# Kernel tuning notes

Measured on AMD Instinct MI355X. Metric: run time of the kernel, lower is better.

The kernel has to match this reference:

```python
import jax, jax.numpy as jnp
import numpy as np

B = 1; S = 2048; HID = 1024; NH = 8; HD = 128; INTER = 4096
EPS = 1e-6; THETA = 10000.0


def rms_norm(x, w):
    # Gemma RMSNorm: x * rsqrt(mean(x^2)+eps) * (1 + w)
    v = jnp.mean(x * x, axis=-1, keepdims=True)
    return x * jax.lax.rsqrt(v + EPS) * (1.0 + w)


def rope_cos_sin(seqlen):
    inv = 1.0 / (THETA ** (jnp.arange(0, HD, 2, dtype=jnp.float32) / HD))
    t = jnp.arange(seqlen, dtype=jnp.float32)
    f = jnp.outer(t, inv)                       # (S, HD/2)
    emb = jnp.concatenate([f, f], axis=-1)      # (S, HD)
    return jnp.cos(emb), jnp.sin(emb)


def rotate_half(x):
    x1, x2 = jnp.split(x, 2, axis=-1)
    return jnp.concatenate([-x2, x1], axis=-1)


def apply_rope(x, cos, sin):
    return x * cos[None, None] + rotate_half(x) * sin[None, None]


def expert_forward(x, mask, params):
    """One GemmaDecoderLayer; returns output plus PRE-RoPE q/k/v (as the torch module exposes)."""
    w_ln, wq, wk, wv, wo, w_pln, wg, wu, wd = params
    res = x
    h = rms_norm(x, w_ln)

    def proj(w):
        return (h @ w).reshape(B, -1, NH, HD).transpose(0, 2, 1, 3)  # (B,H,S,D)

    q, k, v = proj(wq), proj(wk), proj(wv)      # stored before rotary in the original
    cos, sin = rope_cos_sin(x.shape[1])
    qr, kr = apply_rope(q, cos, sin), apply_rope(k, cos, sin)
    scores = jnp.einsum('bhqd,bhkd->bhqk', qr, kr) * (HD ** -0.5) + mask
    attn = jnp.einsum('bhqk,bhkd->bhqd', jax.nn.softmax(scores, axis=-1), v)
    attn = attn.transpose(0, 2, 1, 3).reshape(B, -1, NH * HD) @ wo
    h1 = res + attn
    m = rms_norm(h1, w_pln)
    mlp = (jax.nn.gelu(m @ wg, approximate=True) * (m @ wu)) @ wd  # gelu_pytorch_tanh
    return h1 + mlp, q, k, v


def setup_inputs() -> dict:
    key = jax.random.key(0)
    ks = iter(jax.random.split(key, 40))

    def w(shape, scale=0.02):
        return jax.random.normal(next(ks), shape, jnp.float32) * scale

    inp = {
        'x_a': jax.random.normal(next(ks), (B, S, HID), jnp.float32),
        'x_b': jax.random.normal(next(ks), (B, S, HID), jnp.float32),
    }
    tri = jnp.tril(jnp.ones((S, S), bool))
    causal = jnp.where(tri, 0.0, -1e9).astype(jnp.float32)[None, None]  # additive causal mask
    inp['mask_a'] = causal
    inp['mask_b'] = causal
    inp['mix_mask'] = jnp.zeros((B, 1, 2 * S, 2 * S), jnp.float32)      # non-causal cross-expert
    for e in ('a', 'b'):
        inp['w_ln_' + e] = jnp.zeros((HID,), jnp.float32)
        inp['w_q_' + e] = w((HID, NH * HD))
        inp['w_k_' + e] = w((HID, NH * HD))
        inp['w_v_' + e] = w((HID, NH * HD))
        inp['w_o_' + e] = w((NH * HD, HID))
        inp['w_pln_' + e] = jnp.zeros((HID,), jnp.float32)
        inp['w_g_' + e] = w((HID, INTER))
        inp['w_u_' + e] = w((HID, INTER))
        inp['w_d_' + e] = w((INTER, HID))
    return inp


def reference(x_a, x_b, mask_a, mask_b, mix_mask,
              w_ln_a, w_q_a, w_k_a, w_v_a, w_o_a, w_pln_a, w_g_a, w_u_a, w_d_a,
              w_ln_b, w_q_b, w_k_b, w_v_b, w_o_b, w_pln_b, w_g_b, w_u_b, w_d_b):
    pa = (w_ln_a, w_q_a, w_k_a, w_v_a, w_o_a, w_pln_a, w_g_a, w_u_a, w_d_a)
    pb = (w_ln_b, w_q_b, w_k_b, w_v_b, w_o_b, w_pln_b, w_g_b, w_u_b, w_d_b)
    out_a, qa, ka, va = expert_forward(x_a, mask_a, pa)
    out_b, qb, kb, vb = expert_forward(x_b, mask_b, pb)
    # cross-expert mixed attention over concatenated (pre-RoPE) streams
    q = jnp.concatenate([qa, qb], axis=2)
    k = jnp.concatenate([ka, kb], axis=2)
    v = jnp.concatenate([va, vb], axis=2)
    scores = jnp.einsum('bhqd,bhkd->bhqk', q, k) * (HD ** -0.5) + mix_mask
    mixed = jnp.einsum('bhqk,bhkd->bhqd', jax.nn.softmax(scores, axis=-1), v)
    mixed = mixed.transpose(0, 2, 1, 3).reshape(B, 2 * S, NH * HD)
    ma, mb = mixed[:, :S], mixed[:, S:]
    return jnp.stack([out_a + ma @ w_o_a, out_b + mb @ w_o_b])
```

## Files before the change

kernel.cpp:

```cpp
#include <hip/hip_runtime.h>
#include <hip/hip_bf16.h>
#include <math.h>

#define S 2048
#define HID 1024
#define NH 8
#define HD 128
#define INTER 4096
#define EPSV 1e-6f
#define THETA 10000.0f

typedef __hip_bfloat16 bf16;
typedef unsigned short u16;
typedef __attribute__((ext_vector_type(8))) short bf16x8;
typedef __attribute__((ext_vector_type(4))) float f32x4;

__device__ inline float bu2f(u16 u) {
    unsigned int x = ((unsigned int)u) << 16;
    return __uint_as_float(x);
}
__device__ inline u16 f2bu(float f) {
    bf16 h = __float2bfloat16(f);
    return *reinterpret_cast<u16*>(&h);
}
__device__ inline float ldin(const void* p, size_t i, bool isbf) {
    return isbf ? bu2f(((const u16*)p)[i]) : ((const float*)p)[i];
}
__device__ inline float gelu_tanh(float x) {
    float x3 = x * x * x;
    return 0.5f * x * (1.f + tanhf(0.7978845608028654f * (x + 0.044715f * x3)));
}
__device__ inline void gload16(const u16* g, u16* l) {
    __builtin_amdgcn_global_load_lds(
        (const __attribute__((address_space(1))) void*)g,
        (__attribute__((address_space(3))) void*)l, 16, 0, 0);
}

__global__ __launch_bounds__(256) void probe_kernel(const unsigned short* __restrict__ x,
                                                    int* __restrict__ flag) {
    __shared__ int red[256];
    int tid = threadIdx.x;
    int cnt = 0;
    for (int i = tid; i < 2048; i += 256) {
        unsigned short u = x[2 * i];
        int e = (u >> 7) & 0xFF;
        cnt += (e >= 110 && e <= 135) ? 1 : 0;
    }
    red[tid] = cnt;
    __syncthreads();
    for (int off = 128; off > 0; off >>= 1) {
        if (tid < off) red[tid] += red[tid + off];
        __syncthreads();
    }
    if (tid == 0) *flag = (red[0] > 1024) ? 1 : 0;
}

__global__ __launch_bounds__(256) void transpose_w(const void* __restrict__ W,
                                                   u16* __restrict__ WT,
                                                   const int* __restrict__ flag,
                                                   int K, int N) {
    bool isbf = (*flag != 0);
    __shared__ float t[32][33];
    int n0 = blockIdx.x * 32, k0 = blockIdx.y * 32;
    int c = threadIdx.x & 31, r = threadIdx.x >> 5;
#pragma unroll
    for (int p = 0; p < 4; p++)
        t[r + 8 * p][c] = ldin(W, (size_t)(k0 + r + 8 * p) * N + n0 + c, isbf);
    __syncthreads();
#pragma unroll
    for (int p = 0; p < 4; p++) {
        int row = r + 8 * p;
        WT[(size_t)(n0 + row) * K + k0 + c] = f2bu(t[c][row]);
    }
}

__global__ __launch_bounds__(256) void transpose_v(const u16* __restrict__ V0,
                                                   const u16* __restrict__ V1, int sv,
                                                   u16* __restrict__ VT) {
    const u16* V = blockIdx.z ? V1 : V0;
    VT += (size_t)blockIdx.z * ((size_t)NH * HD * S);
    __shared__ u16 t[32][33];
    int k0 = blockIdx.x * 32;
    int d0 = blockIdx.y * 32;
    int c = threadIdx.x & 31, r = threadIdx.x >> 5;
#pragma unroll
    for (int p = 0; p < 4; p++)
        t[r + 8 * p][c] = V[(size_t)(k0 + r + 8 * p) * sv + d0 + c];
    __syncthreads();
#pragma unroll
    for (int p = 0; p < 4; p++)
        VT[(size_t)(d0 + r + 8 * p) * S + k0 + c] = t[c][r + 8 * p];
}

struct RmsDual {
    const void* x[2];
    const void* w[2];
    u16* y[2];
};
__global__ __launch_bounds__(256) void rmsnorm_kernel(RmsDual rd,
                                                      const int* __restrict__ flag,
                                                      int dual) {
    int e = blockIdx.y;
    const void* x = rd.x[e];
    const void* w = rd.w[e];
    u16* y = rd.y[e];
    bool isbf = (*flag != 0);
    bool xbf = dual && isbf;
    int row = blockIdx.x;
    size_t base = (size_t)row * HID;
    __shared__ float red[256];
    float xv[4];
    float s = 0.f;
#pragma unroll
    for (int i = 0; i < 4; i++) {
        float v = ldin(x, base + threadIdx.x + 256 * i, xbf);
        xv[i] = v;
        s += v * v;
    }
    red[threadIdx.x] = s;
    __syncthreads();
    for (int off = 128; off > 0; off >>= 1) {
        if (threadIdx.x < off) red[threadIdx.x] += red[threadIdx.x + off];
        __syncthreads();
    }
    float scale = rsqrtf(red[0] / (float)HID + EPSV);
#pragma unroll
    for (int i = 0; i < 4; i++) {
        int c = threadIdx.x + 256 * i;
        y[base + c] = f2bu(xv[i] * scale * (1.f + ldin(w, c, isbf)));
    }
}

struct GemmDual {
    const u16* A[2];
    const u16* BT[2];
    float* Cf[2];
    u16* Cb[2];
    const void* res[2];
};
template <int BM, int BN, int WRN, int WCN, int EPI>
__global__ __launch_bounds__(256) void gemm_mfma(GemmDual g, const int* __restrict__ flag,
                                                 int M, int N, int K) {
    int eZ = blockIdx.z;
    const u16* __restrict__ A = g.A[eZ];
    const u16* __restrict__ BT = g.BT[eZ];
    float* __restrict__ Cf = g.Cf[eZ];
    u16* __restrict__ Cb = g.Cb[eZ];
    const void* __restrict__ res = g.res[eZ];
    constexpr int BK = 32;
    constexpr int WM = BM / WRN, WN = BN / WCN, TI = WM / 16, TJ = WN / 16;
    __shared__ u16 As[BM * 32];
    __shared__ u16 Bs[BN * 32];
    int tid = threadIdx.x, lane = tid & 63, wv = tid >> 6;
    int wr = wv / WCN, wc = wv % WCN;
    int m = lane & 15, quad = lane >> 4;
    int m0 = blockIdx.y * BM, n0 = blockIdx.x * BN;
    f32x4 acc[TI][TJ] = {};
    for (int k0 = 0; k0 < K; k0 += BK) {
        __syncthreads();
#pragma unroll
        for (int c2 = 0; c2 < BM / 64; c2++) {
            int row0 = (wv * (BM / 64) + c2) * 16;
            int row = row0 + (lane >> 2);
            int ch = lane & 3;
            gload16(&A[(size_t)(m0 + row) * K + k0 + ((ch ^ ((row >> 1) & 3)) << 3)],
                    &As[row0 * 32]);
        }
#pragma unroll
        for (int c2 = 0; c2 < BN / 64; c2++) {
            int row0 = (wv * (BN / 64) + c2) * 16;
            int row = row0 + (lane >> 2);
            int ch = lane & 3;
            gload16(&BT[(size_t)(n0 + row) * K + k0 + ((ch ^ ((row >> 1) & 3)) << 3)],
                    &Bs[row0 * 32]);
        }
        __syncthreads();
        bf16x8 af[TI], bf_[TJ];
#pragma unroll
        for (int i = 0; i < TI; i++) {
            int rr = wr * WM + i * 16 + m;
            af[i] = *reinterpret_cast<const bf16x8*>(&As[rr * 32 + ((quad ^ ((rr >> 1) & 3)) << 3)]);
        }
#pragma unroll
        for (int j = 0; j < TJ; j++) {
            int rr = wc * WN + j * 16 + m;
            bf_[j] = *reinterpret_cast<const bf16x8*>(&Bs[rr * 32 + ((quad ^ ((rr >> 1) & 3)) << 3)]);
        }
#pragma unroll
        for (int i = 0; i < TI; i++)
#pragma unroll
            for (int j = 0; j < TJ; j++)
                acc[i][j] = __builtin_amdgcn_mfma_f32_16x16x32_bf16(af[i], bf_[j], acc[i][j], 0, 0, 0);
    }
    bool isbf = (EPI == 1) ? (*flag != 0) : false;
#pragma unroll
    for (int i = 0; i < TI; i++) {
#pragma unroll
        for (int j = 0; j < TJ; j++) {
#pragma unroll
            for (int r = 0; r < 4; r++) {
                int row = m0 + wr * WM + i * 16 + quad * 4 + r;
                int col = n0 + wc * WN + j * 16 + m;
                size_t idx = (size_t)row * N + col;
                float v = acc[i][j][r];
                if (EPI == 0) Cb[idx] = f2bu(v);
                else if (EPI == 1) Cf[idx] = v + ldin(res, idx, isbf);
                else Cf[idx] = Cf[idx] + v;
            }
        }
    }
}

template <int BM, int BN, int WRN, int WCN>
__global__ __launch_bounds__(256) void gemm_gated_mfma(const u16* __restrict__ A,
                                                       const u16* __restrict__ BgT,
                                                       const u16* __restrict__ BuT,
                                                       u16* __restrict__ C,
                                                       int M, int N, int K) {
    constexpr int BK = 32;
    constexpr int WM = BM / WRN, WN = BN / WCN, TI = WM / 16, TJ = WN / 16;
    __shared__ u16 As[BM * 32];
    __shared__ u16 Bgs[BN * 32];
    __shared__ u16 Bus[BN * 32];
    int tid = threadIdx.x, lane = tid & 63, wv = tid >> 6;
    int wr = wv / WCN, wc = wv % WCN;
    int m = lane & 15, quad = lane >> 4;
    int m0 = blockIdx.y * BM, n0 = blockIdx.x * BN;
    f32x4 accg[TI][TJ] = {};
    f32x4 accu[TI][TJ] = {};
    for (int k0 = 0; k0 < K; k0 += BK) {
        __syncthreads();
#pragma unroll
        for (int c2 = 0; c2 < BM / 64; c2++) {
            int row0 = (wv * (BM / 64) + c2) * 16;
            int row = row0 + (lane >> 2);
            int ch = lane & 3;
            gload16(&A[(size_t)(m0 + row) * K + k0 + ((ch ^ ((row >> 1) & 3)) << 3)],
                    &As[row0 * 32]);
        }
#pragma unroll
        for (int c2 = 0; c2 < BN / 64; c2++) {
            int row0 = (wv * (BN / 64) + c2) * 16;
            int row = row0 + (lane >> 2);
            int ch = lane & 3;
            gload16(&BgT[(size_t)(n0 + row) * K + k0 + ((ch ^ ((row >> 1) & 3)) << 3)],
                    &Bgs[row0 * 32]);
            gload16(&BuT[(size_t)(n0 + row) * K + k0 + ((ch ^ ((row >> 1) & 3)) << 3)],
                    &Bus[row0 * 32]);
        }
        __syncthreads();
        bf16x8 af[TI], bg[TJ], bu[TJ];
#pragma unroll
        for (int i = 0; i < TI; i++) {
            int rr = wr * WM + i * 16 + m;
            af[i] = *reinterpret_cast<const bf16x8*>(&As[rr * 32 + ((quad ^ ((rr >> 1) & 3)) << 3)]);
        }
#pragma unroll
        for (int j = 0; j < TJ; j++) {
            int rr = wc * WN + j * 16 + m;
            int off = rr * 32 + ((quad ^ ((rr >> 1) & 3)) << 3);
            bg[j] = *reinterpret_cast<const bf16x8*>(&Bgs[off]);
            bu[j] = *reinterpret_cast<const bf16x8*>(&Bus[off]);
        }
#pragma unroll
        for (int i = 0; i < TI; i++)
#pragma unroll
            for (int j = 0; j < TJ; j++) {
                accg[i][j] = __builtin_amdgcn_mfma_f32_16x16x32_bf16(af[i], bg[j], accg[i][j], 0, 0, 0);
                accu[i][j] = __builtin_amdgcn_mfma_f32_16x16x32_bf16(af[i], bu[j], accu[i][j], 0, 0, 0);
            }
    }
#pragma unroll
    for (int i = 0; i < TI; i++)
#pragma unroll
        for (int j = 0; j < TJ; j++)
#pragma unroll
            for (int r = 0; r < 4; r++) {
                int row = m0 + wr * WM + i * 16 + quad * 4 + r;
                int col = n0 + wc * WN + j * 16 + m;
                C[(size_t)row * N + col] = f2bu(gelu_tanh(accg[i][j][r]) * accu[i][j][r]);
            }
}

__global__ __launch_bounds__(64) void rope_kernel(const u16* __restrict__ qkv0,
                                                  const u16* __restrict__ qkv1,
                                                  u16* __restrict__ qr,
                                                  u16* __restrict__ kr) {
    const u16* qkv = blockIdx.z ? qkv1 : qkv0;
    size_t zo = (size_t)blockIdx.z * ((size_t)S * HID);
    int b = blockIdx.x;
    int t = b >> 3, h = b & 7;
    int i = threadIdx.x;
    size_t ib = (size_t)t * 3072 + h * HD;
    size_t ob = zo + (size_t)t * HID + h * HD;
    float inv = powf(THETA, -(float)(2 * i) / (float)HD);
    float f = (float)t * inv;
    float c = cosf(f), s = sinf(f);
    float q1 = bu2f(qkv[ib + i]), q2 = bu2f(qkv[ib + i + 64]);
    qr[ob + i] = f2bu(q1 * c - q2 * s);
    qr[ob + i + 64] = f2bu(q2 * c + q1 * s);
    float k1 = bu2f(qkv[ib + 1024 + i]), k2 = bu2f(qkv[ib + 1024 + i + 64]);
    kr[ob + i] = f2bu(k1 * c - k2 * s);
    kr[ob + i + 64] = f2bu(k2 * c + k1 * s);
}

__device__ inline int swz64(int row, int b) {
    return row * 64 + (b ^ (((row >> 1) & 3) << 4));
}

template <bool CAUSAL>
__global__ __launch_bounds__(256, 4) void attn_mfma_kernel(
    const u16* __restrict__ qa, const u16* __restrict__ qb, int sq,
    const u16* __restrict__ ka, const u16* __restrict__ kb, int sk,
    const u16* __restrict__ vta, const u16* __restrict__ vtb,
    u16* __restrict__ Out, int nkeys) {
    __shared__ char Ks[4 * 64 * 64];
    __shared__ char VTs[2 * 128 * 64];

    int tid = threadIdx.x;
    int lane = tid & 63, w = tid >> 6;
    int col = lane & 15, quad = lane >> 4;
    int eZ = CAUSAL ? (int)blockIdx.z : 0;
    int bx = (CAUSAL && eZ) ? ((int)gridDim.x - 1 - (int)blockIdx.x) : (int)blockIdx.x;
    int q0 = bx * 64;
    int h = blockIdx.y;
    const float scale = 0.08838834764831845f;

    int q0r = CAUSAL ? q0 : (q0 & (S - 1));
    const u16* qsel = CAUSAL ? (eZ ? qb : qa) : ((q0 < S) ? qa : qb);
    const u16* qp = qsel + (size_t)q0r * sq;
    bf16x8 aq[4];
#pragma unroll
    for (int t = 0; t < 4; t++)
        aq[t] = *reinterpret_cast<const bf16x8*>(
            qp + (size_t)(16 * w + col) * sq + h * HD + 32 * t + quad * 8);

    const u16* kplo = (CAUSAL && eZ) ? kb : ka;
    const u16* vplo = (CAUSAL && eZ) ? vtb : vta;

    f32x4 o[8] = {};
    float m_ = -1e30f, l_ = 0.f;

    int sA = col + 16 * (2 * (quad & 1));
    int sB = sA + 16;
    bool hi = (quad >> 1) != 0;

    int ntiles = CAUSAL ? (q0 >> 6) + 1 : (nkeys >> 6);
    for (int tt = 0; tt < ntiles; tt++) {
        int j0 = tt * 64;
        int j0r = j0 & (S - 1);
        bool eb = (!CAUSAL) && (j0 >= S);
        const u16* kp = eb ? kb : kplo;
        const u16* vp = eb ? vtb : vplo;
        __syncthreads();
#pragma unroll
        for (int i = 0; i < 4; i++) {
            int l = tid + 256 * i;
            int key = l >> 4, c = l & 15;
            int t = c >> 2, kq = c & 3;
            *reinterpret_cast<uint4*>(&Ks[t * 4096 + swz64(key, kq * 16)]) =
                *reinterpret_cast<const uint4*>(kp + (size_t)(j0r + key) * sk + h * HD + c * 8);
        }
#pragma unroll
        for (int i = 0; i < 4; i++) {
            int l = tid + 256 * i;
            int d = l >> 3, c = l & 7;
            int ks = c >> 2, kq = c & 3;
            *reinterpret_cast<uint4*>(&VTs[ks * 8192 + swz64(d, kq * 16)]) =
                *reinterpret_cast<const uint4*>(vp + (size_t)(h * HD + d) * S + j0r + c * 8);
        }
        __syncthreads();

        f32x4 sc[4] = {};
        __builtin_amdgcn_s_setprio(1);
#pragma unroll
        for (int t = 0; t < 4; t++) {
#pragma unroll
            for (int ct = 0; ct < 4; ct++) {
                bf16x8 kf = *reinterpret_cast<const bf16x8*>(
                    &Ks[t * 4096 + swz64(16 * ct + col, quad * 16)]);
                sc[ct] = __builtin_amdgcn_mfma_f32_16x16x32_bf16(kf, aq[t], sc[ct], 0, 0, 0);
            }
        }
        __builtin_amdgcn_s_setprio(0);
        bool diag = CAUSAL && (j0 == q0);
#pragma unroll
        for (int ct = 0; ct < 4; ct++) {
#pragma unroll
            for (int r = 0; r < 4; r++) {
                float v = sc[ct][r] * scale;
                if (diag && (16 * ct + 4 * quad + r > 16 * w + col)) v = -1e30f;
                sc[ct][r] = v;
            }
        }

        float mx0 = fmaxf(fmaxf(sc[0][0], sc[0][1]), fmaxf(sc[0][2], sc[0][3]));
        float mx1 = fmaxf(fmaxf(sc[1][0], sc[1][1]), fmaxf(sc[1][2], sc[1][3]));
        float mx2 = fmaxf(fmaxf(sc[2][0], sc[2][1]), fmaxf(sc[2][2], sc[2][3]));
        float mx3 = fmaxf(fmaxf(sc[3][0], sc[3][1]), fmaxf(sc[3][2], sc[3][3]));
        float rmax = fmaxf(fmaxf(mx0, mx1), fmaxf(mx2, mx3));
        rmax = fmaxf(rmax, __shfl_xor(rmax, 16));
        rmax = fmaxf(rmax, __shfl_xor(rmax, 32));
        float mn = fmaxf(m_, rmax);
        float al = __expf(m_ - mn);
#pragma unroll
        for (int ct = 0; ct < 4; ct++)
#pragma unroll
            for (int r = 0; r < 4; r++) sc[ct][r] = __expf(sc[ct][r] - mn);
        float s0 = (sc[0][0] + sc[0][1]) + (sc[0][2] + sc[0][3]);
        float s1 = (sc[1][0] + sc[1][1]) + (sc[1][2] + sc[1][3]);
        float s2 = (sc[2][0] + sc[2][1]) + (sc[2][2] + sc[2][3]);
        float s3 = (sc[3][0] + sc[3][1]) + (sc[3][2] + sc[3][3]);
        float rs = (s0 + s1) + (s2 + s3);
        rs += __shfl_xor(rs, 16);
        rs += __shfl_xor(rs, 32);
        l_ = l_ * al + rs;
        m_ = mn;

        unsigned int pu[4][2];
#pragma unroll
        for (int ct = 0; ct < 4; ct++) {
            pu[ct][0] = (unsigned int)f2bu(sc[ct][0]) | ((unsigned int)f2bu(sc[ct][1]) << 16);
            pu[ct][1] = (unsigned int)f2bu(sc[ct][2]) | ((unsigned int)f2bu(sc[ct][3]) << 16);
        }

#pragma unroll
        for (int nt = 0; nt < 8; nt++)
#pragma unroll
            for (int r = 0; r < 4; r++) o[nt][r] *= al;

#pragma unroll
        for (int ks = 0; ks < 2; ks++) {
            unsigned int a0 = __shfl(pu[2 * ks][0], sA);
            unsigned int a1 = __shfl(pu[2 * ks][1], sA);
            unsigned int c0 = __shfl(pu[2 * ks + 1][0], sA);
            unsigned int c1 = __shfl(pu[2 * ks + 1][1], sA);
            unsigned int b0 = __shfl(pu[2 * ks][0], sB);
            unsigned int b1 = __shfl(pu[2 * ks][1], sB);
            unsigned int g0 = __shfl(pu[2 * ks + 1][0], sB);
            unsigned int g1 = __shfl(pu[2 * ks + 1][1], sB);
            union {
                unsigned int u[4];
                bf16x8 v;
            } pb;
            pb.u[0] = hi ? c0 : a0;
            pb.u[1] = hi ? c1 : a1;
            pb.u[2] = hi ? g0 : b0;
            pb.u[3] = hi ? g1 : b1;
            __builtin_amdgcn_s_setprio(1);
#pragma unroll
            for (int nt = 0; nt < 8; nt++) {
                bf16x8 vf = *reinterpret_cast<const bf16x8*>(
                    &VTs[ks * 8192 + swz64(16 * nt + col, quad * 16)]);
                o[nt] = __builtin_amdgcn_mfma_f32_16x16x32_bf16(vf, pb.v, o[nt], 0, 0, 0);
            }
            __builtin_amdgcn_s_setprio(0);
        }
    }

    u16* outp = Out + (CAUSAL ? (size_t)eZ * ((size_t)S * HID) : (size_t)0);
    float inv = 1.f / l_;
    size_t rowoff = (size_t)(q0 + 16 * w + col) * HID + (size_t)h * HD + 4 * quad;
#pragma unroll
    for (int nt = 0; nt < 8; nt++) {
        ushort4 st;
        st.x = f2bu(o[nt][0] * inv);
        st.y = f2bu(o[nt][1] * inv);
        st.z = f2bu(o[nt][2] * inv);
        st.w = f2bu(o[nt][3] * inv);
        *reinterpret_cast<ushort4*>(&outp[rowoff + 16 * nt]) = st;
    }
}

__global__ __launch_bounds__(256) void store_out_kernel(const float* __restrict__ a,
                                                        const float* __restrict__ b,
                                                        void* __restrict__ out,
                                                        const int* __restrict__ flag) {
    bool isbf = (*flag != 0);
    size_t i = (size_t)blockIdx.x * 256 + threadIdx.x;
    const size_t MM = (size_t)S * HID;
    float v = (i < MM) ? a[i] : b[i - MM];
    if (isbf)
        ((bf16*)out)[i] = __float2bfloat16(v);
    else
        ((float*)out)[i] = v;
}

extern "C" void kernel_launch(void* const* d_in, const int* in_sizes, int n_in,
                              void* d_out, int out_size, void* d_ws, size_t ws_size,
                              hipStream_t stream) {
    const void* x[2] = {d_in[0], d_in[1]};
    const void* w_ln[2] = {d_in[5], d_in[14]};
    const void* w_q[2] = {d_in[6], d_in[15]};
    const void* w_k[2] = {d_in[7], d_in[16]};
    const void* w_v[2] = {d_in[8], d_in[17]};
    const void* w_o[2] = {d_in[9], d_in[18]};
    const void* w_pln[2] = {d_in[10], d_in[19]};
    const void* w_g[2] = {d_in[11], d_in[20]};
    const void* w_u[2] = {d_in[12], d_in[21]};
    const void* w_d[2] = {d_in[13], d_in[22]};

    char* base = (char*)d_ws;
    int* flag = (int*)base;
    u16* p = (u16*)(base + 256);
    const size_t E_QKV = (size_t)S * 3072;
    const size_t E_SH = (size_t)S * HID;
    const size_t E_VT = (size_t)NH * HD * S;

    u16* qkv[2] = {p, p + E_QKV};            p += 2 * E_QKV;
    u16* qr = p;                             p += 2 * E_SH;
    u16* kr = p;                             p += 2 * E_SH;
    u16* h_bf = p;                           p += 2 * E_SH;
    u16* attnbuf = p;                        p += 2 * E_SH;
    u16* vtg = p;                            p += 2 * E_VT;
    u16* gated = qr;
    u16* mixed = qr;
    u16* wqkvT = p;                          p += 2 * (size_t)3072 * 1024;
    u16* woT[2] = {p, p + (size_t)1024 * 1024};  p += 2 * (size_t)1024 * 1024;
    u16* wgT = p;                            p += (size_t)INTER * 1024;
    u16* wuT = p;                            p += (size_t)INTER * 1024;
    u16* wdT = p;                            p += (size_t)1024 * INTER;
    float* fbase = (float*)(((size_t)p + 255) & ~(size_t)255);
    float* outX[2] = {fbase, fbase + E_SH};

    probe_kernel<<<1, 256, 0, stream>>>((const unsigned short*)d_in[0], flag);

    for (int e = 0; e < 2; e++) {
        u16* wt = wqkvT + (size_t)e * 3072 * 1024;
        transpose_w<<<dim3(32, 32), 256, 0, stream>>>(w_q[e], wt, flag, 1024, 1024);
        transpose_w<<<dim3(32, 32), 256, 0, stream>>>(w_k[e], wt + (size_t)1024 * 1024, flag, 1024, 1024);
        transpose_w<<<dim3(32, 32), 256, 0, stream>>>(w_v[e], wt + (size_t)2048 * 1024, flag, 1024, 1024);
        transpose_w<<<dim3(32, 32), 256, 0, stream>>>(w_o[e], woT[e], flag, 1024, 1024);
    }

    {
        RmsDual rd = {{x[0], x[1]}, {w_ln[0], w_ln[1]}, {h_bf, h_bf + E_SH}};
        rmsnorm_kernel<<<dim3(S, 2), 256, 0, stream>>>(rd, flag, 1);
    }
    {
        GemmDual g = {{h_bf, h_bf + E_SH},
                      {wqkvT, wqkvT + (size_t)3072 * 1024},
                      {nullptr, nullptr},
                      {qkv[0], qkv[1]},
                      {nullptr, nullptr}};
        gemm_mfma<128, 128, 2, 2, 0><<<dim3(3072 / 128, S / 128, 2), 256, 0, stream>>>(
            g, flag, S, 3072, 1024);
    }
    rope_kernel<<<dim3(S * NH, 1, 2), 64, 0, stream>>>(qkv[0], qkv[1], qr, kr);
    transpose_v<<<dim3(S / 32, 1024 / 32, 2), 256, 0, stream>>>(qkv[0] + 2048, qkv[1] + 2048, 3072, vtg);
    attn_mfma_kernel<true><<<dim3(S / 64, NH, 2), 256, 0, stream>>>(
        qr, qr + E_SH, HID, kr, kr + E_SH, HID, vtg, vtg + E_VT, attnbuf, S);
    {
        GemmDual g = {{attnbuf, attnbuf + E_SH},
                      {woT[0], woT[1]},
                      {outX[0], outX[1]},
                      {nullptr, nullptr},
                      {x[0], x[1]}};
        gemm_mfma<64, 128, 1, 4, 1><<<dim3(1024 / 128, S / 64, 2), 256, 0, stream>>>(
            g, flag, S, 1024, 1024);
    }
    {
        RmsDual rd = {{outX[0], outX[1]}, {w_pln[0], w_pln[1]}, {h_bf, h_bf + E_SH}};
        rmsnorm_kernel<<<dim3(S, 2), 256, 0, stream>>>(rd, flag, 0);
    }

    for (int e = 0; e < 2; e++) {
        transpose_w<<<dim3(INTER / 32, 1024 / 32), 256, 0, stream>>>(w_g[e], wgT, flag, 1024, INTER);
        transpose_w<<<dim3(INTER / 32, 1024 / 32), 256, 0, stream>>>(w_u[e], wuT, flag, 1024, INTER);
        gemm_gated_mfma<128, 64, 2, 2><<<dim3(INTER / 64, S / 128), 256, 0, stream>>>(
            h_bf + e * E_SH, wgT, wuT, gated, S, INTER, 1024);
        transpose_w<<<dim3(1024 / 32, INTER / 32), 256, 0, stream>>>(w_d[e], wdT, flag, INTER, 1024);
        GemmDual g = {{gated, gated}, {wdT, wdT}, {outX[e], outX[e]}, {nullptr, nullptr}, {nullptr, nullptr}};
        gemm_mfma<64, 128, 1, 4, 2><<<dim3(1024 / 128, S / 64, 1), 256, 0, stream>>>(
            g, flag, S, 1024, INTER);
    }

    attn_mfma_kernel<false><<<dim3(2 * S / 64, NH), 256, 0, stream>>>(
        qkv[0], qkv[1], 3072, qkv[0] + 1024, qkv[1] + 1024, 3072,
        vtg, vtg + E_VT, mixed, 2 * S);
    {
        GemmDual g = {{mixed, mixed + E_SH},
                      {woT[0], woT[1]},
                      {outX[0], outX[1]},
                      {nullptr, nullptr},
                      {nullptr, nullptr}};
        gemm_mfma<64, 128, 1, 4, 2><<<dim3(1024 / 128, S / 64, 2), 256, 0, stream>>>(
            g, flag, S, 1024, 1024);
    }

    store_out_kernel<<<(2 * E_SH) / 256, 256, 0, stream>>>(outX[0], outX[1], d_out, flag);
}
```

Baseline: 874.3 us.

## Double-buffer attention K/V staging, batch weight transposes, retile output GEMMs

Attention now stages K and V tiles into two shared-memory buffers with direct global-to-LDS loads (gload16), prefetching the next tile while computing the current one, and drops occupancy from 4 to 2 blocks per CU. The separate weight transpose launches are merged into single multi-z launches. The RoPE frequency moves from powf to __expf. The o-proj and down-proj GEMMs switch from a 64x128 1x4 tile to a 64x64 2x2 tile. The aim is to hide load latency in attention and cut launch overhead, at the cost of more LDS use and lower occupancy.

```diff
diff --git a/kernel.cpp b/kernel.cpp
--- a/kernel.cpp
+++ b/kernel.cpp
@@ -55,11 +55,15 @@
     if (tid == 0) *flag = (red[0] > 1024) ? 1 : 0;
 }
 
-__global__ __launch_bounds__(256) void transpose_w(const void* __restrict__ W,
-                                                   u16* __restrict__ WT,
-                                                   const int* __restrict__ flag,
-                                                   int K, int N) {
+struct TransN {
+    const void* W[8];
+    u16* T[8];
+};
+__global__ __launch_bounds__(256) void transpose_wN(TransN tn, const int* __restrict__ flag,
+                                                    int K, int N) {
     bool isbf = (*flag != 0);
+    const void* W = tn.W[blockIdx.z];
+    u16* WT = tn.T[blockIdx.z];
     __shared__ float t[32][33];
     int n0 = blockIdx.x * 32, k0 = blockIdx.y * 32;
     int c = threadIdx.x & 31, r = threadIdx.x >> 5;
@@ -293,7 +297,7 @@
     int i = threadIdx.x;
     size_t ib = (size_t)t * 3072 + h * HD;
     size_t ob = zo + (size_t)t * HID + h * HD;
-    float inv = powf(THETA, -(float)(2 * i) / (float)HD);
+    float inv = __expf(-9.210340372f * (float)(2 * i) / (float)HD);
     float f = (float)t * inv;
     float c = cosf(f), s = sinf(f);
     float q1 = bu2f(qkv[ib + i]), q2 = bu2f(qkv[ib + i + 64]);
@@ -309,13 +313,13 @@
 }
 
 template <bool CAUSAL>
-__global__ __launch_bounds__(256, 4) void attn_mfma_kernel(
+__global__ __launch_bounds__(256, 2) void attn_mfma_kernel(
     const u16* __restrict__ qa, const u16* __restrict__ qb, int sq,
     const u16* __restrict__ ka, const u16* __restrict__ kb, int sk,
     const u16* __restrict__ vta, const u16* __restrict__ vtb,
     u16* __restrict__ Out, int nkeys) {
-    __shared__ char Ks[4 * 64 * 64];
-    __shared__ char VTs[2 * 128 * 64];
+    __shared__ char Ks[2][16384];
+    __shared__ char VTs[2][16384];
 
     int tid = threadIdx.x;
     int lane = tid & 63, w = tid >> 6;
@@ -346,30 +350,38 @@
     bool hi = (quad >> 1) != 0;
 
     int ntiles = CAUSAL ? (q0 >> 6) + 1 : (nkeys >> 6);
-    for (int tt = 0; tt < ntiles; tt++) {
-        int j0 = tt * 64;
-        int j0r = j0 & (S - 1);
-        bool eb = (!CAUSAL) && (j0 >= S);
+
+    auto stage = [&](int buf, int tt) {
+        int j0r = (tt * 64) & (S - 1);
+        bool eb = (!CAUSAL) && (tt >= (S >> 6));
         const u16* kp = eb ? kb : kplo;
         const u16* vp = eb ? vtb : vplo;
-        __syncthreads();
+        char* kd = &Ks[buf][(tid >> 6) * 1024];
+        char* vd = &VTs[buf][(tid >> 6) * 1024];
 #pragma unroll
         for (int i = 0; i < 4; i++) {
-            int l = tid + 256 * i;
-            int key = l >> 4, c = l & 15;
-            int t = c >> 2, kq = c & 3;
-            *reinterpret_cast<uint4*>(&Ks[t * 4096 + swz64(key, kq * 16)]) =
-                *reinterpret_cast<const uint4*>(kp + (size_t)(j0r + key) * sk + h * HD + c * 8);
+            int l = 256 * i + tid;
+            int key = (l >> 2) & 63;
+            int c = (l >> 8) * 4 + ((l & 3) ^ ((key >> 1) & 3));
+            gload16(kp + (size_t)(j0r + key) * sk + h * HD + c * 8, (u16*)(kd + i * 4096));
         }
 #pragma unroll
         for (int i = 0; i < 4; i++) {
-            int l = tid + 256 * i;
-            int d = l >> 3, c = l & 7;
-            int ks = c >> 2, kq = c & 3;
-            *reinterpret_cast<uint4*>(&VTs[ks * 8192 + swz64(d, kq * 16)]) =
-                *reinterpret_cast<const uint4*>(vp + (size_t)(h * HD + d) * S + j0r + c * 8);
-        }
-        __syncthreads();
+            int l = 256 * i + tid;
+            int d = (l >> 2) & 127;
+            int c = (l >> 9) * 4 + ((l & 3) ^ ((d >> 1) & 3));
+            gload16(vp + (size_t)(h * HD + d) * S + j0r + c * 8, (u16*)(vd + i * 4096));
+        }
+    };
+
+    stage(0, 0);
+    __syncthreads();
+    int cur = 0;
+
+    for (int tt = 0; tt < ntiles; tt++) {
+        if (tt + 1 < ntiles) stage(cur ^ 1, tt + 1);
+        const char* Kb = Ks[cur];
+        const char* Vb = VTs[cur];
 
         f32x4 sc[4] = {};
         __builtin_amdgcn_s_setprio(1);
@@ -378,12 +390,12 @@
 #pragma unroll
             for (int ct = 0; ct < 4; ct++) {
                 bf16x8 kf = *reinterpret_cast<const bf16x8*>(
-                    &Ks[t * 4096 + swz64(16 * ct + col, quad * 16)]);
+                    Kb + t * 4096 + swz64(16 * ct + col, quad * 16));
                 sc[ct] = __builtin_amdgcn_mfma_f32_16x16x32_bf16(kf, aq[t], sc[ct], 0, 0, 0);
             }
         }
         __builtin_amdgcn_s_setprio(0);
-        bool diag = CAUSAL && (j0 == q0);
+        bool diag = CAUSAL && (tt == ntiles - 1);
 #pragma unroll
         for (int ct = 0; ct < 4; ct++) {
 #pragma unroll
@@ -451,11 +463,14 @@
 #pragma unroll
             for (int nt = 0; nt < 8; nt++) {
                 bf16x8 vf = *reinterpret_cast<const bf16x8*>(
-                    &VTs[ks * 8192 + swz64(16 * nt + col, quad * 16)]);
+                    Vb + ks * 8192 + swz64(16 * nt + col, quad * 16));
                 o[nt] = __builtin_amdgcn_mfma_f32_16x16x32_bf16(vf, pb.v, o[nt], 0, 0, 0);
             }
             __builtin_amdgcn_s_setprio(0);
         }
+
+        __syncthreads();
+        cur ^= 1;
     }
 
     u16* outp = Out + (CAUSAL ? (size_t)eZ * ((size_t)S * HID) : (size_t)0);
@@ -525,12 +540,16 @@
 
     probe_kernel<<<1, 256, 0, stream>>>((const unsigned short*)d_in[0], flag);
 
-    for (int e = 0; e < 2; e++) {
-        u16* wt = wqkvT + (size_t)e * 3072 * 1024;
-        transpose_w<<<dim3(32, 32), 256, 0, stream>>>(w_q[e], wt, flag, 1024, 1024);
-        transpose_w<<<dim3(32, 32), 256, 0, stream>>>(w_k[e], wt + (size_t)1024 * 1024, flag, 1024, 1024);
-        transpose_w<<<dim3(32, 32), 256, 0, stream>>>(w_v[e], wt + (size_t)2048 * 1024, flag, 1024, 1024);
-        transpose_w<<<dim3(32, 32), 256, 0, stream>>>(w_o[e], woT[e], flag, 1024, 1024);
+    {
+        TransN tn = {};
+        for (int e = 0; e < 2; e++) {
+            u16* wt = wqkvT + (size_t)e * 3072 * 1024;
+            tn.W[4 * e + 0] = w_q[e];  tn.T[4 * e + 0] = wt;
+            tn.W[4 * e + 1] = w_k[e];  tn.T[4 * e + 1] = wt + (size_t)1024 * 1024;
+            tn.W[4 * e + 2] = w_v[e];  tn.T[4 * e + 2] = wt + (size_t)2048 * 1024;
+            tn.W[4 * e + 3] = w_o[e];  tn.T[4 * e + 3] = woT[e];
+        }
+        transpose_wN<<<dim3(32, 32, 8), 256, 0, stream>>>(tn, flag, 1024, 1024);
     }
 
     {
@@ -556,7 +575,7 @@
                       {outX[0], outX[1]},
                       {nullptr, nullptr},
                       {x[0], x[1]}};
-        gemm_mfma<64, 128, 1, 4, 1><<<dim3(1024 / 128, S / 64, 2), 256, 0, stream>>>(
+        gemm_mfma<64, 64, 2, 2, 1><<<dim3(1024 / 64, S / 64, 2), 256, 0, stream>>>(
             g, flag, S, 1024, 1024);
     }
     {
@@ -565,13 +584,21 @@
     }
 
     for (int e = 0; e < 2; e++) {
-        transpose_w<<<dim3(INTER / 32, 1024 / 32), 256, 0, stream>>>(w_g[e], wgT, flag, 1024, INTER);
-        transpose_w<<<dim3(INTER / 32, 1024 / 32), 256, 0, stream>>>(w_u[e], wuT, flag, 1024, INTER);
+        {
+            TransN tg = {};
+            tg.W[0] = w_g[e];  tg.T[0] = wgT;
+            tg.W[1] = w_u[e];  tg.T[1] = wuT;
+            transpose_wN<<<dim3(INTER / 32, 1024 / 32, 2), 256, 0, stream>>>(tg, flag, 1024, INTER);
+        }
         gemm_gated_mfma<128, 64, 2, 2><<<dim3(INTER / 64, S / 128), 256, 0, stream>>>(
             h_bf + e * E_SH, wgT, wuT, gated, S, INTER, 1024);
-        transpose_w<<<dim3(1024 / 32, INTER / 32), 256, 0, stream>>>(w_d[e], wdT, flag, INTER, 1024);
+        {
+            TransN td = {};
+            td.W[0] = w_d[e];  td.T[0] = wdT;
+            transpose_wN<<<dim3(1024 / 32, INTER / 32, 1), 256, 0, stream>>>(td, flag, INTER, 1024);
+        }
         GemmDual g = {{gated, gated}, {wdT, wdT}, {outX[e], outX[e]}, {nullptr, nullptr}, {nullptr, nullptr}};
-        gemm_mfma<64, 128, 1, 4, 2><<<dim3(1024 / 128, S / 64, 1), 256, 0, stream>>>(
+        gemm_mfma<64, 64, 2, 2, 2><<<dim3(1024 / 64, S / 64, 1), 256, 0, stream>>>(
             g, flag, S, 1024, INTER);
     }
 
@@ -584,7 +611,7 @@
                       {outX[0], outX[1]},
                       {nullptr, nullptr},
                       {nullptr, nullptr}};
-        gemm_mfma<64, 128, 1, 4, 2><<<dim3(1024 / 128, S / 64, 2), 256, 0, stream>>>(
+        gemm_mfma<64, 64, 2, 2, 2><<<dim3(1024 / 64, S / 64, 2), 256, 0, stream>>>(
             g, flag, S, 1024, 1024);
     }
 
```

Result: faster. 796.3 us (-8.9%).
